# Kernel tuning notes

Hardware: AMD Instinct MI355X
Metric: run time of the kernel (lower is better)

Reference implementation:

```python
import jax, jax.numpy as jnp
import numpy as np

K = 3          # B-spline order (cubic)
G = 10         # number of spline intervals over [0, 1]
NELY, NELX = 512, 512
WIDTHS = [2, 32, 32, 1]


def _make_grid(in_dim):
    # extended uniform knot vector over [0,1] with K extra knots each side: (in_dim, G+2K+1)
    h = 1.0 / G
    knots = jnp.arange(-K, G + K + 1, dtype=jnp.float32) * h
    return jnp.tile(knots[None, :], (in_dim, 1))


def setup_inputs() -> dict:
    key = jax.random.key(0)
    ks = jax.random.split(key, 1 + 3 * (len(WIDTHS) - 1))
    inp = {"coords": jax.random.uniform(ks[0], (NELY * NELX, 2), dtype=jnp.float32)}
    for l, (i, o) in enumerate(zip(WIDTHS[:-1], WIDTHS[1:])):
        inp[f"grid{l}"] = _make_grid(i)
        inp[f"coef{l}"] = 0.1 * jax.random.normal(ks[1 + 3 * l], (i, o, G + K), dtype=jnp.float32)
        inp[f"sb{l}"] = jax.random.normal(ks[2 + 3 * l], (i, o), dtype=jnp.float32) / np.sqrt(i).astype(np.float32)
        inp[f"sp{l}"] = jnp.ones((i, o), dtype=jnp.float32)
    inp["density_bias"] = jnp.full((1,), np.float32(np.log(0.5 / (1.0 - 0.5 + 1e-8))))
    return inp


def _b_batch(x, grid):
    # Cox-de Boor recursion. x: (B, in), grid: (in, G+2K+1) -> bases (B, in, G+K)
    xe = x[:, :, None]
    v = ((xe >= grid[None, :, :-1]) & (xe < grid[None, :, 1:])).astype(x.dtype)
    for p in range(1, K + 1):
        left = (xe - grid[None, :, : -(p + 1)]) / (grid[None, :, p:-1] - grid[None, :, : -(p + 1)])
        right = (grid[None, :, p + 1:] - xe) / (grid[None, :, p + 1:] - grid[None, :, 1:-p])
        v = left * v[:, :, :-1] + right * v[:, :, 1:]
    return v


def _kan_layer(x, grid, coef, sb, sp):
    # y_out = sum_in [ sb * silu(x) + sp * sum_k B_k(x) * coef_k ]
    B = _b_batch(x, grid)                               # (batch, in, G+K)
    spline = jnp.einsum('bik,iok->bio', B, coef)        # (batch, in, out)
    base = jax.nn.silu(x)                               # (batch, in)
    return jnp.sum(sb[None] * base[:, :, None] + sp[None] * spline, axis=1)


def reference(coords, grid0, coef0, sb0, sp0, grid1, coef1, sb1, sp1,
              grid2, coef2, sb2, sp2, density_bias):
    h = _kan_layer(coords, grid0, coef0, sb0, sp0)
    h = _kan_layer(h, grid1, coef1, sb1, sp1)
    logits = _kan_layer(h, grid2, coef2, sb2, sp2) + density_bias
    return jax.nn.sigmoid(logits).reshape(1, NELY, NELX)
```

## Files before the change

### kernel.cpp

```cpp
#include <hip/hip_runtime.h>
#include <hip/hip_bf16.h>

typedef __hip_bfloat16 bf16;
typedef __fp16 h2v __attribute__((ext_vector_type(2)));
typedef __fp16 half8 __attribute__((ext_vector_type(8)));
typedef float floatx4 __attribute__((ext_vector_type(4)));

#define NPTS (512*512)

#define OFF_BIAS 12
#define OFF_FLAG 13
#define OFF_BF   16
#define NFRAG    34
#define OFF_PP   (16 + NFRAG*256)
#define PP_WORDS (32*18*4)
#define OFF_SB2  (OFF_PP + PP_WORDS)
#define SB2_WORDS 32
#define STAGE_WORDS (PP_WORDS + SB2_WORDS)


__device__ __forceinline__ bool sniff_f32(const void* g0) {
    float f = ((const float*)g0)[0];
    return fabsf(f + 0.3f) < 0.01f;
}
__device__ __forceinline__ float ld(const void* p, int i, bool f32) {
    return f32 ? ((const float*)p)[i] : __bfloat162float(((const bf16*)p)[i]);
}
__device__ __forceinline__ unsigned pk_rtn(float a, float b) {
    union { h2v v; unsigned u; } x;
    x.v[0] = (__fp16)a; x.v[1] = (__fp16)b;
    return x.u;
}
__device__ __forceinline__ unsigned pkf16(float a, float b) {
    union { h2v v; unsigned u; } x;
    x.v = __builtin_amdgcn_cvt_pkrtz(a, b);
    return x.u;
}

__device__ float slotval(int layer, int K, int o,
                         const void* c0, const void* sb0, const void* sp0,
                         const void* c1, const void* sb1, const void* sp1,
                         bool f32)
{
    int i = K >> 4, s = K & 15;
    if (s >= 1 && s <= 13) {
        int m = s - 1;
        if (layer == 0) return ld(c0, (i*32+o)*13 + m, f32) * ld(sp0, i*32+o, f32);
        return ld(c1, (i*32+o)*13 + m, f32) * ld(sp1, i*32+o, f32);
    }
    if (s == 14) {
        if (layer == 0) return ld(sb0, i*32+o, f32);
        return ld(sb1, i*32+o, f32);
    }
    return 0.0f;
}

__global__ __launch_bounds__(256) void kan_prep(
    const void* __restrict__ g0, const void* __restrict__ c0,
    const void* __restrict__ sb0, const void* __restrict__ sp0,
    const void* __restrict__ g1, const void* __restrict__ c1,
    const void* __restrict__ sb1, const void* __restrict__ sp1,
    const void* __restrict__ g2, const void* __restrict__ c2,
    const void* __restrict__ sb2, const void* __restrict__ sp2,
    const void* __restrict__ bias, float* __restrict__ ws)
{
    const bool f32 = sniff_f32(g0);
    int t = blockIdx.x * blockDim.x + threadIdx.x;

    if (t < 16) {
        if (t < 12) {
            int l = t >> 2, j = t & 3;
            const void* g = (l == 0) ? g0 : (l == 1) ? g1 : g2;
            float lo = ld(g, 0, f32), hi = ld(g, 16, f32);
            float ih = 16.0f / (hi - lo);
            float v = (j == 0) ? lo : (j == 1) ? hi
                    : (j == 2) ? ih : (-lo * ih);
            ws[t] = v;
        } else if (t == 12) ws[12] = ld(bias, 0, f32);
        else if (t == 13)   ws[13] = f32 ? 1.0f : 0.0f;
        else                ws[t] = 0.0f;
        return;
    }
    int ft = t - 16;
    if (ft < NFRAG * 64) {
        int f = ft >> 6, l = ft & 63, n = l & 15, q = l >> 4;
        int layer, c, nt;
        if (f < 2) { layer = 0; c = 0;            nt = f; }
        else       { layer = 1; c = (f - 2) >> 1; nt = (f - 2) & 1; }
        int o = nt * 16 + n;
        unsigned wv[4];
#pragma unroll
        for (int jp = 0; jp < 4; jp++) {
            int K0 = c * 32 + q * 8 + jp * 2;
            float v0 = slotval(layer, K0,     o, c0,sb0,sp0, c1,sb1,sp1, f32);
            float v1 = slotval(layer, K0 + 1, o, c0,sb0,sp0, c1,sb1,sp1, f32);
            wv[jp] = pk_rtn(v0, v1);
        }
        uint4 out4; out4.x = wv[0]; out4.y = wv[1]; out4.z = wv[2]; out4.w = wv[3];
        ((uint4*)((unsigned*)ws + OFF_BF))[f * 64 + l] = out4;
        return;
    }
    int e = ft - NFRAG * 64;
    if (e < 32 * 18) {
        int i = e / 18, seg = e - i * 18, jc = seg - 1;
        float L[4];
#pragma unroll
        for (int k = 0; k < 4; k++) {
            int j = jc + k;
            L[k] = (j >= 3 && j <= 15)
                 ? ld(c2, i*13 + (j - 3), f32) * ld(sp2, i, f32) : 0.0f;
        }
        const float s6 = 0.166666667f;
        float a3 = (-L[0] + 3.0f*L[1] - 3.0f*L[2] + L[3]) * s6;
        float a2 = ( 3.0f*L[0] - 6.0f*L[1] + 3.0f*L[2]) * s6;
        float a1 = (-3.0f*L[0] + 3.0f*L[2]) * s6;
        float a0 = ( L[0] + 4.0f*L[1] + L[2]) * s6;
        float4 out4; out4.x = a3; out4.y = a2; out4.z = a1; out4.w = a0;
        ((float4*)(ws + OFF_PP))[e] = out4;
        return;
    }
    int sbi = e - 32 * 18;
    if (sbi < SB2_WORDS) {
        ws[OFF_SB2 + sbi] = ld(sb2, sbi, f32);
    }
}

__device__ __forceinline__ floatx4 mf(uint4 a, uint4 b, floatx4 c)
{
    union { uint4 u; half8 h; } ua, ub;
    ua.u = a; ub.u = b;
    return __builtin_amdgcn_mfma_f32_16x16x32_f16(ua.h, ub.h, c, 0, 0, 0);
}

__device__ __forceinline__ void eval_taps(float x, float ngh, float ih,
    unsigned& A, unsigned& B, unsigned& C, int& wout, float& si)
{
    float t  = fmaf(x, ih, ngh);
    float fj = floorf(t);
    float u  = t - fj;
    bool inb = (t >= 0.0f) && (t < 16.0f);
    float s6 = inb ? 0.166666667f : 0.0f;
    int jc = min(max((int)fj, 0), 15);
    float u2 = u * u, u3 = u2 * u, om = 1.0f - u;
    float b0 = om * om * om * s6;
    float b1 = (fmaf(3.0f, u3, 4.0f) - 6.0f * u2) * s6;
    float b2 = fmaf(-3.0f, u3, fmaf(3.0f, u2, fmaf(3.0f, u, 1.0f))) * s6;
    float b3 = u3 * s6;
    int s0 = jc - 2;
    wout = ((s0 + 2) >> 1) - 1;
    if (s0 & 1) { A = pkf16(0.0f, b0); B = pkf16(b1, b2); C = pkf16(b3, 0.0f); }
    else        { A = pkf16(b0, b1);   B = pkf16(b2, b3); C = 0u; }
    si = x / (1.0f + __expf(-x));
}

struct Tap1 { unsigned A, B, C, S; int w; };

__device__ __forceinline__ Tap1 eval1(float x, float ngh, float ih)
{
    Tap1 t; float si;
    eval_taps(x, ngh, ih, t.A, t.B, t.C, t.w, si);
    t.S = pkf16(si, 0.0f);
    return t;
}

__device__ __forceinline__ void commit32(unsigned* row, int hb, const Tap1& t)
{
    uint4 z; z.x = 0u; z.y = 0u; z.z = 0u; z.w = 0u;
    *(uint4*)(row + hb)     = z;
    *(uint4*)(row + hb + 4) = z;
    int base = hb + t.w;
    row[base + 2] = t.C;
    row[base + 1] = t.B;
    row[base < 0 ? 18 : base] = t.A;
    row[hb + 7] = t.S;
}

__global__ __launch_bounds__(256, 4) void kan_main(
    const void* __restrict__ coords, const float* __restrict__ ws,
    void* __restrict__ out)
{
    __shared__ __align__(16) unsigned lds[4 * 640 + STAGE_WORDS];
    const unsigned* wsu = (const unsigned*)ws;
    const uint4* bfp = (const uint4*)(wsu + OFF_BF);

    int tid = threadIdx.x;
    int l = tid & 63, w = tid >> 6;
    int pt = l & 31, hf = l >> 5;
    int p = blockIdx.x * 128 + w * 32 + pt;

    unsigned* pps = lds + 4 * 640;
#pragma unroll
    for (int j = 0; j < 10; j++) {
        int idx = tid + j * 256;
        if (idx < STAGE_WORDS) pps[idx] = wsu[OFF_PP + idx];
    }
    __syncthreads();

    unsigned* rb = lds + w * 640;
    unsigned* cb = rb;
    unsigned* myrow = cb + pt * 20;
    const int hb = hf * 8;

    const bool f32 = (ws[OFF_FLAG] != 0.0f);
    float x0, x1;
    if (f32) {
        float2 c = ((const float2*)coords)[p];
        x0 = c.x; x1 = c.y;
    } else {
        unsigned cc = ((const unsigned*)coords)[p];
        union { unsigned u; float f; } cv;
        cv.u = (cc & 0xffffu) << 16;  x0 = cv.f;
        cv.u = cc & 0xffff0000u;      x1 = cv.f;
    }

    const float iha = ws[2],  ngha = ws[3];
    const float ihb = ws[6],  nghb = ws[7];
    const float ihc = ws[10], nghc = ws[11];

    const int arow = l & 15, aq = (l >> 4) * 4;
    const int drow = (l >> 4) * 4, dcol = l & 15;

    float h[32];

    {
        floatx4 acc[2][2];
#pragma unroll
        for (int mt = 0; mt < 2; mt++)
#pragma unroll
            for (int nt = 0; nt < 2; nt++) acc[mt][nt] = (floatx4)0.0f;

        uint4 bf0 = bfp[0 * 64 + l], bf1 = bfp[1 * 64 + l];
        Tap1 t0 = eval1(hf ? x1 : x0, ngha, iha);
        commit32(myrow, hb, t0);
#pragma unroll
        for (int mt = 0; mt < 2; mt++) {
            uint4 a = *(const uint4*)(cb + (arow + 16 * mt) * 20 + aq);
            acc[mt][0] = mf(a, bf0, acc[mt][0]);
            acc[mt][1] = mf(a, bf1, acc[mt][1]);
        }
#pragma unroll
        for (int nt = 0; nt < 2; nt++) {
#pragma unroll
            for (int mt = 0; mt < 2; mt++)
#pragma unroll
                for (int r = 0; r < 4; r++)
                    rb[(mt*16 + drow + r) * 20 + dcol] =
                        __float_as_uint(acc[mt][nt][r]);
#pragma unroll
            for (int q = 0; q < 4; q++) {
                uint4 v = *(const uint4*)(rb + pt * 20 + q * 4);
                h[nt*16 + q*4+0] = __uint_as_float(v.x);
                h[nt*16 + q*4+1] = __uint_as_float(v.y);
                h[nt*16 + q*4+2] = __uint_as_float(v.z);
                h[nt*16 + q*4+3] = __uint_as_float(v.w);
            }
        }
    }

    {
        floatx4 acc[2][2];
#pragma unroll
        for (int mt = 0; mt < 2; mt++)
#pragma unroll
            for (int nt = 0; nt < 2; nt++) acc[mt][nt] = (floatx4)0.0f;

#pragma unroll
        for (int c = 0; c < 16; c++) {
            uint4 bf0 = bfp[(2 + 2*c) * 64 + l];
            uint4 bf1 = bfp[(3 + 2*c) * 64 + l];
            float xf = hf ? h[2*c + 1] : h[2*c];
            Tap1 tn = eval1(xf, nghb, ihb);
            commit32(myrow, hb, tn);
#pragma unroll
            for (int mt = 0; mt < 2; mt++) {
                uint4 a = *(const uint4*)(cb + (arow + 16 * mt) * 20 + aq);
                acc[mt][0] = mf(a, bf0, acc[mt][0]);
                acc[mt][1] = mf(a, bf1, acc[mt][1]);
            }
        }
#pragma unroll
        for (int nt = 0; nt < 2; nt++) {
#pragma unroll
            for (int mt = 0; mt < 2; mt++)
#pragma unroll
                for (int r = 0; r < 4; r++)
                    rb[(mt*16 + drow + r) * 20 + dcol] =
                        __float_as_uint(acc[mt][nt][r]);
#pragma unroll
            for (int q = 0; q < 4; q++) {
                uint4 v = *(const uint4*)(rb + pt * 20 + q * 4);
                h[nt*16 + q*4+0] = __uint_as_float(v.x);
                h[nt*16 + q*4+1] = __uint_as_float(v.y);
                h[nt*16 + q*4+2] = __uint_as_float(v.z);
                h[nt*16 + q*4+3] = __uint_as_float(v.w);
            }
        }
    }

    {
        const float* ppt = (const float*)pps;
        const float* sbt = (const float*)(pps + PP_WORDS);
        const int ibase = hf * 16;
        float z0 = 0.0f, z1 = 0.0f;
#pragma unroll
        for (int i = 0; i < 16; i++) {
            float x = hf ? h[16 + i] : h[i];
            float t  = fmaf(x, ihc, nghc);
            float fj = floorf(t);
            float u  = t - fj;
            int seg = min(max((int)fj, -1), 16) + 1;
            const float* pr = ppt + ((ibase + i) * 18 + seg) * 4;
            float4 a = *(const float4*)pr;
            float pv = fmaf(fmaf(fmaf(a.x, u, a.y), u, a.z), u, a.w);
            float si = x / (1.0f + __expf(-x));
            z0 += pv;
            z1 = fmaf(si, sbt[ibase + i], z1);
        }
        float z = z0 + z1;
        z += __shfl_xor(z, 32);
        z += ws[OFF_BIAS];
        float r = 1.0f / (1.0f + __expf(-z));
        if (hf == 0) {
            if (f32) ((float*)out)[p] = r;
            else     ((bf16*)out)[p] = __float2bfloat16(r);
        }
    }
}

extern "C" void kernel_launch(void* const* d_in, const int* in_sizes, int n_in,
                              void* d_out, int out_size, void* d_ws, size_t ws_size,
                              hipStream_t stream)
{
    float* ws = (float*)d_ws;

    kan_prep<<<(16 + NFRAG*64 + 32*18 + SB2_WORDS + 255) / 256, 256, 0, stream>>>(
        d_in[1], d_in[2], d_in[3], d_in[4],
        d_in[5], d_in[6], d_in[7], d_in[8],
        d_in[9], d_in[10], d_in[11], d_in[12],
        d_in[13], ws);

    kan_main<<<NPTS / 128, 256, 0, stream>>>(d_in[0], ws, d_out);
}
```

Measured before the change: 108.7 us.

## Build MFMA A-fragments in registers with permlane16 swap instead of LDS

Replaces the LDS round-trip used to build the MFMA A operand from per-lane spline taps. Each lane now assembles its 8-word tap row in registers with selects, and the halves are exchanged across lanes with permlane16_swap to form the two M-tile fragments directly. This removes LDS stores, loads and the implied waitcnts from each layer-1 and layer-2 step. The cost is extra select instructions and cross-lane permute ops, and it relies on the permlane lane mapping matching the fragment layout.

```diff
diff --git a/kernel.cpp b/kernel.cpp
--- a/kernel.cpp
+++ b/kernel.cpp
@@ -5,6 +5,7 @@
 typedef __fp16 h2v __attribute__((ext_vector_type(2)));
 typedef __fp16 half8 __attribute__((ext_vector_type(8)));
 typedef float floatx4 __attribute__((ext_vector_type(4)));
+typedef unsigned uint2v __attribute__((ext_vector_type(2)));
 
 #define NPTS (512*512)
 
@@ -163,16 +164,28 @@
     return t;
 }
 
-__device__ __forceinline__ void commit32(unsigned* row, int hb, const Tap1& t)
-{
-    uint4 z; z.x = 0u; z.y = 0u; z.z = 0u; z.w = 0u;
-    *(uint4*)(row + hb)     = z;
-    *(uint4*)(row + hb + 4) = z;
-    int base = hb + t.w;
-    row[base + 2] = t.C;
-    row[base + 1] = t.B;
-    row[base < 0 ? 18 : base] = t.A;
-    row[hb + 7] = t.S;
+__device__ __forceinline__ void composef(const Tap1& t, uint4& lo, uint4& hi)
+{
+    const int wv = t.w;
+    lo.x = (wv == 0) ? t.A : ((wv == -1) ? t.B : 0u);
+    lo.y = (wv == 1) ? t.A : ((wv ==  0) ? t.B : ((wv == -1) ? t.C : 0u));
+    lo.z = (wv == 2) ? t.A : ((wv ==  1) ? t.B : ((wv ==  0) ? t.C : 0u));
+    lo.w = (wv == 3) ? t.A : ((wv ==  2) ? t.B : ((wv ==  1) ? t.C : 0u));
+    hi.x = (wv == 4) ? t.A : ((wv ==  3) ? t.B : ((wv ==  2) ? t.C : 0u));
+    hi.y = (wv == 5) ? t.A : ((wv ==  4) ? t.B : ((wv ==  3) ? t.C : 0u));
+    hi.z = (wv == 6) ? t.A : ((wv ==  5) ? t.B : ((wv ==  4) ? t.C : 0u));
+    hi.w = t.S;
+}
+
+__device__ __forceinline__ void swapfrag(uint4 lo, uint4 hi,
+                                         uint4& f0, uint4& f1)
+{
+    uint2v r0 = __builtin_amdgcn_permlane16_swap(lo.x, hi.x, false, false);
+    uint2v r1 = __builtin_amdgcn_permlane16_swap(lo.y, hi.y, false, false);
+    uint2v r2 = __builtin_amdgcn_permlane16_swap(lo.z, hi.z, false, false);
+    uint2v r3 = __builtin_amdgcn_permlane16_swap(lo.w, hi.w, false, false);
+    f0.x = r0[0]; f0.y = r1[0]; f0.z = r2[0]; f0.w = r3[0];
+    f1.x = r0[1]; f1.y = r1[1]; f1.z = r2[1]; f1.w = r3[1];
 }
 
 __global__ __launch_bounds__(256, 4) void kan_main(
@@ -197,9 +210,6 @@
     __syncthreads();
 
     unsigned* rb = lds + w * 640;
-    unsigned* cb = rb;
-    unsigned* myrow = cb + pt * 20;
-    const int hb = hf * 8;
 
     const bool f32 = (ws[OFF_FLAG] != 0.0f);
     float x0, x1;
@@ -217,7 +227,6 @@
     const float ihb = ws[6],  nghb = ws[7];
     const float ihc = ws[10], nghc = ws[11];
 
-    const int arow = l & 15, aq = (l >> 4) * 4;
     const int drow = (l >> 4) * 4, dcol = l & 15;
 
     float h[32];
@@ -231,13 +240,13 @@
 
         uint4 bf0 = bfp[0 * 64 + l], bf1 = bfp[1 * 64 + l];
         Tap1 t0 = eval1(hf ? x1 : x0, ngha, iha);
-        commit32(myrow, hb, t0);
-#pragma unroll
-        for (int mt = 0; mt < 2; mt++) {
-            uint4 a = *(const uint4*)(cb + (arow + 16 * mt) * 20 + aq);
-            acc[mt][0] = mf(a, bf0, acc[mt][0]);
-            acc[mt][1] = mf(a, bf1, acc[mt][1]);
-        }
+        uint4 lo, hi, fa0, fa1;
+        composef(t0, lo, hi);
+        swapfrag(lo, hi, fa0, fa1);
+        acc[0][0] = mf(fa0, bf0, acc[0][0]);
+        acc[0][1] = mf(fa0, bf1, acc[0][1]);
+        acc[1][0] = mf(fa1, bf0, acc[1][0]);
+        acc[1][1] = mf(fa1, bf1, acc[1][1]);
 #pragma unroll
         for (int nt = 0; nt < 2; nt++) {
 #pragma unroll
@@ -270,13 +279,13 @@
             uint4 bf1 = bfp[(3 + 2*c) * 64 + l];
             float xf = hf ? h[2*c + 1] : h[2*c];
             Tap1 tn = eval1(xf, nghb, ihb);
-            commit32(myrow, hb, tn);
-#pragma unroll
-            for (int mt = 0; mt < 2; mt++) {
-                uint4 a = *(const uint4*)(cb + (arow + 16 * mt) * 20 + aq);
-                acc[mt][0] = mf(a, bf0, acc[mt][0]);
-                acc[mt][1] = mf(a, bf1, acc[mt][1]);
-            }
+            uint4 lo, hi, fa0, fa1;
+            composef(tn, lo, hi);
+            swapfrag(lo, hi, fa0, fa1);
+            acc[0][0] = mf(fa0, bf0, acc[0][0]);
+            acc[0][1] = mf(fa0, bf1, acc[0][1]);
+            acc[1][0] = mf(fa1, bf0, acc[1][0]);
+            acc[1][1] = mf(fa1, bf1, acc[1][1]);
         }
 #pragma unroll
         for (int nt = 0; nt < 2; nt++) {
```

After: 111.7 us. 1.03x slower.
